# Kernel optimization log

Hardware: AMD Instinct MI355X
Metric: run time of the kernel (lower is better)

The kernel has to match this reference:

```python
import jax, jax.numpy as jnp
import numpy as np

PARTS_NUM = 16
MAX_INIT = -100.0  # torch scatter_reduce amax include_self initial value


def setup_inputs() -> dict:
    key = jax.random.key(0)
    k1, k2 = jax.random.split(key)
    x = jax.random.normal(k1, (32, 256, 30, 16, 16), dtype=jnp.float32)
    part_labels = jax.random.randint(k2, (32, 30, 16, 16), 0, PARTS_NUM, dtype=jnp.int64)
    return {"x": x, "part_labels": part_labels}


def reference(x, part_labels):
    n, c, s, h, w = x.shape
    ns = n * s
    hw = h * w
    P = PARTS_NUM
    # feat: (ns*hw, c) -- channels-last for efficient segment reductions
    feat = jnp.transpose(x, (0, 2, 3, 4, 1)).reshape(ns * hw, c)
    labels = part_labels.reshape(ns, hw).astype(jnp.int32)
    # one flat segment id per (frame, part) pair
    seg = (labels + jnp.arange(ns, dtype=jnp.int32)[:, None] * P).reshape(ns * hw)
    num_seg = ns * P
    pooled_sum = jax.ops.segment_sum(feat, seg, num_segments=num_seg)          # (ns*P, c)
    pooled_count = jax.ops.segment_sum(jnp.ones((ns * hw,), feat.dtype), seg,
                                       num_segments=num_seg)                   # (ns*P,)
    pooled_max = jax.ops.segment_max(feat, seg, num_segments=num_seg)          # (ns*P, c)
    valid = (pooled_count > 0)[:, None]                                        # (ns*P, 1)
    pooled_mean = pooled_sum / jnp.maximum(pooled_count, 1.0)[:, None]
    # torch scatter_reduce includes initial -100.0 in the amax; empty parts -> 0
    pooled_max = jnp.where(valid, jnp.maximum(pooled_max, MAX_INIT), 0.0)
    pooled = pooled_mean + pooled_max                                          # (ns*P, c)
    # -> (n, c, s, P)
    return jnp.transpose(pooled.reshape(n, s, P, c), (0, 3, 1, 2))
```

## Files before the change

### kernel.cpp

```cpp
#include <hip/hip_runtime.h>


#define C_DIM 256
#define S_DIM 30
#define P_NUM 16
#define HW 256
#define CH_PER_BLK 32
#define TS 260

__global__ __launch_bounds__(256, 4)
void partpp_pool_kernel(const float* __restrict__ x,
                        const int* __restrict__ labels,
                        float* __restrict__ out) {
    __shared__ float tile[CH_PER_BLK * TS];
    __shared__ int rank[HW];
    __shared__ int counts[P_NUM], cursor[P_NUM], offs[P_NUM + 1];

    const int t   = threadIdx.x;
    const int b   = blockIdx.x;
    const int f   = b >> 3;
    const int q   = b & 7;
    const int ch0 = q * CH_PER_BLK;
    const int n   = f / S_DIM;
    const int s   = f - n * S_DIM;

    const int lab = labels[f * HW + t];

    const size_t xbase = ((size_t)(n * C_DIM + ch0) * S_DIM + s) * HW;
    const int col = t & 63;
    float4 v[8];
    #pragma unroll
    for (int j = 0; j < 8; ++j) {
        const int row = j * 4 + (t >> 6);
        v[j] = *(const float4*)(x + xbase + (size_t)row * (S_DIM * HW) + col * 4);
    }

    if (t < P_NUM) { counts[t] = 0; cursor[t] = 0; }
    __syncthreads();
    atomicAdd(&counts[lab], 1);
    __syncthreads();
    if (t == 0) {
        int acc = 0;
        #pragma unroll
        for (int p = 0; p < P_NUM; ++p) { offs[p] = acc; acc += counts[p]; }
        offs[P_NUM] = acc;
    }
    __syncthreads();
    rank[t] = offs[lab] + atomicAdd(&cursor[lab], 1);
    __syncthreads();

    const int4 rk = *(const int4*)&rank[col * 4];
    #pragma unroll
    for (int j = 0; j < 8; ++j) {
        const int row = j * 4 + (t >> 6);
        float* rp = &tile[row * TS];
        rp[rk.x] = v[j].x;
        rp[rk.y] = v[j].y;
        rp[rk.z] = v[j].z;
        rp[rk.w] = v[j].w;
    }
    __syncthreads();

    const int ch  = t >> 3;
    const int sub = t & 7;
    const float* rowp = &tile[ch * TS];

    float res[2];
    #pragma unroll
    for (int pi = 0; pi < 2; ++pi) {
        const int p  = sub * 2 + pi;
        const int jb = offs[p];
        const int je = offs[p + 1];
        float sum = 0.0f;
        float mx  = -3.0e38f;
        for (int j = jb; j < je; ++j) {
            const float vv = rowp[j];
            sum += vv;
            mx = fmaxf(mx, vv);
        }
        res[pi] = (je > jb) ? (sum / (float)(je - jb) + fmaxf(mx, -100.0f)) : 0.0f;
    }

    float* op = out + ((size_t)(n * C_DIM + ch0 + ch) * S_DIM + s) * P_NUM + sub * 2;
    *(float2*)op = make_float2(res[0], res[1]);
}

extern "C" void kernel_launch(void* const* d_in, const int* in_sizes, int n_in,
                              void* d_out, int out_size, void* d_ws, size_t ws_size,
                              hipStream_t stream) {
    const float* x      = (const float*)d_in[0];
    const int*   labels = (const int*)d_in[1];
    float*       out    = (float*)d_out;

    dim3 grid(960 * 8), block(256);
    hipLaunchKernelGGL(partpp_pool_kernel, grid, block, 0, stream, x, labels, out);
}
```

Baseline: 336.7 us.

## Precompute per-frame label ranks and offsets in a separate metadata kernel

Splits the label counting-sort (counts, prefix offsets, ranks) into a small preliminary kernel that runs once per frame and writes ranks and offsets to workspace. The pooling kernel then reads precomputed ranks instead of redoing the histogram with shared atomics and several barriers in each of the eight channel blocks per frame. This removes redundant work and synchronisation from the main kernel at the cost of an extra launch and a round trip of rank data through global memory.

```diff
diff --git a/kernel.cpp b/kernel.cpp
--- a/kernel.cpp
+++ b/kernel.cpp
@@ -8,35 +8,17 @@
 #define CH_PER_BLK 32
 #define TS 260
 
-__global__ __launch_bounds__(256, 4)
-void partpp_pool_kernel(const float* __restrict__ x,
-                        const int* __restrict__ labels,
-                        float* __restrict__ out) {
-    __shared__ float tile[CH_PER_BLK * TS];
-    __shared__ int rank[HW];
+__global__ __launch_bounds__(256)
+void partpp_meta_kernel(const int* __restrict__ labels,
+                        int* __restrict__ rank_g,
+                        int* __restrict__ offs_g) {
     __shared__ int counts[P_NUM], cursor[P_NUM], offs[P_NUM + 1];
-
-    const int t   = threadIdx.x;
-    const int b   = blockIdx.x;
-    const int f   = b >> 3;
-    const int q   = b & 7;
-    const int ch0 = q * CH_PER_BLK;
-    const int n   = f / S_DIM;
-    const int s   = f - n * S_DIM;
-
-    const int lab = labels[f * HW + t];
-
-    const size_t xbase = ((size_t)(n * C_DIM + ch0) * S_DIM + s) * HW;
-    const int col = t & 63;
-    float4 v[8];
-    #pragma unroll
-    for (int j = 0; j < 8; ++j) {
-        const int row = j * 4 + (t >> 6);
-        v[j] = *(const float4*)(x + xbase + (size_t)row * (S_DIM * HW) + col * 4);
-    }
+    const int t = threadIdx.x;
+    const int f = blockIdx.x;
 
     if (t < P_NUM) { counts[t] = 0; cursor[t] = 0; }
     __syncthreads();
+    const int lab = labels[f * HW + t];
     atomicAdd(&counts[lab], 1);
     __syncthreads();
     if (t == 0) {
@@ -46,13 +28,42 @@
         offs[P_NUM] = acc;
     }
     __syncthreads();
-    rank[t] = offs[lab] + atomicAdd(&cursor[lab], 1);
-    __syncthreads();
+    rank_g[f * HW + t] = offs[lab] + atomicAdd(&cursor[lab], 1);
+    if (t < P_NUM + 1) offs_g[f * 32 + t] = offs[t];
+}
 
-    const int4 rk = *(const int4*)&rank[col * 4];
+__global__ __launch_bounds__(256, 4)
+void partpp_pool_kernel(const float* __restrict__ x,
+                        const int* __restrict__ rank_g,
+                        const int* __restrict__ offs_g,
+                        float* __restrict__ out) {
+    __shared__ float tile[CH_PER_BLK * TS];
+    __shared__ int offs_sh[P_NUM + 1];
+
+    const int t   = threadIdx.x;
+    const int b   = blockIdx.x;
+    const int f   = b >> 3;
+    const int q   = b & 7;
+    const int ch0 = q * CH_PER_BLK;
+    const int n   = f / S_DIM;
+    const int s   = f - n * S_DIM;
+    const int col = t & 63;
+    const int w   = t >> 6;
+
+    const int4 rk = ((const int4*)(rank_g + f * HW))[col];
+
+    const size_t xbase = ((size_t)(n * C_DIM + ch0) * S_DIM + s) * HW;
+    float4 v[8];
     #pragma unroll
     for (int j = 0; j < 8; ++j) {
-        const int row = j * 4 + (t >> 6);
+        const int row = j * 4 + w;
+        v[j] = *(const float4*)(x + xbase + (size_t)row * (S_DIM * HW) + col * 4);
+    }
+    if (t < P_NUM + 1) offs_sh[t] = offs_g[f * 32 + t];
+
+    #pragma unroll
+    for (int j = 0; j < 8; ++j) {
+        const int row = j * 4 + w;
         float* rp = &tile[row * TS];
         rp[rk.x] = v[j].x;
         rp[rk.y] = v[j].y;
@@ -69,8 +80,8 @@
     #pragma unroll
     for (int pi = 0; pi < 2; ++pi) {
         const int p  = sub * 2 + pi;
-        const int jb = offs[p];
-        const int je = offs[p + 1];
+        const int jb = offs_sh[p];
+        const int je = offs_sh[p + 1];
         float sum = 0.0f;
         float mx  = -3.0e38f;
         for (int j = jb; j < je; ++j) {
@@ -92,6 +103,11 @@
     const int*   labels = (const int*)d_in[1];
     float*       out    = (float*)d_out;
 
-    dim3 grid(960 * 8), block(256);
-    hipLaunchKernelGGL(partpp_pool_kernel, grid, block, 0, stream, x, labels, out);
+    int* rank_g = (int*)d_ws;
+    int* offs_g = rank_g + 960 * HW;
+
+    hipLaunchKernelGGL(partpp_meta_kernel, dim3(960), dim3(256), 0, stream,
+                       labels, rank_g, offs_g);
+    hipLaunchKernelGGL(partpp_pool_kernel, dim3(960 * 8), dim3(256), 0, stream,
+                       x, rank_g, offs_g, out);
 }
```

Result: no change. 339.7 us (+0.9%).
